# Kernel tuning notes

Measured on AMD Instinct MI355X. Metric: run time of the kernel, lower is better.

Reference implementation:

```python
import jax, jax.numpy as jnp
import numpy as np

N = 100_000   # nodes
E = 1_600_000 # edges (avg degree 16)
D0, D1, D2 = 128, 64, 64


def _linp(key, n_out, n_in):
    kw, kb = jax.random.split(key)
    s = 1.0 / np.sqrt(n_in)
    W = jax.random.uniform(kw, (n_out, n_in), jnp.float32, -s, s)
    b = jax.random.uniform(kb, (n_out,), jnp.float32, -s, s)
    return W, b


def setup_inputs() -> dict:
    key = jax.random.key(0)
    ks = jax.random.split(key, 9)
    h = jax.random.normal(ks[0], (N, D0), jnp.float32)
    # guarantee every row has at least one edge (avoids empty-row softmax / 0-std NaNs)
    rows = jnp.concatenate([jnp.arange(N, dtype=jnp.int32),
                            jax.random.randint(ks[1], (E - N,), 0, N, jnp.int32)])
    cols = jax.random.randint(ks[2], (E,), 0, N, jnp.int32)
    edge_index = jnp.stack([rows, cols])  # [2, E], row = softmax segment
    W11, b11 = _linp(ks[3], D1, D0)
    W12, b12 = _linp(ks[4], 1, D1)
    W13, b13 = _linp(ks[5], D1, D0)
    W21, b21 = _linp(ks[6], D2, D1)
    W22, b22 = _linp(ks[7], 1, D2)
    W23, b23 = _linp(ks[8], D2, D1)
    return dict(h=h, edge_index=edge_index,
                W11=W11, b11=b11, W12=W12, b12=b12, W13=W13, b13=b13,
                W21=W21, b21=b21, W22=W22, b22=b22, W23=W23, b23=b23)


def reference(h, edge_index, W11, b11, W12, b12, W13, b13,
              W21, b21, W22, b22, W23, b23):
    src, dst = edge_index[0], edge_index[1]

    def gat_layer(x, Wa, ba, We, be, Wv, bv):
        a = jnp.tanh(x @ Wa.T + ba)                       # [N, d] node scores (l11/l21)
        e = jnp.tanh((a[src] + a[dst]) @ We.T + be)[:, 0] # [E] per-edge logit (l12/l22)
        # per-row (segment) softmax over src = row index
        m = jax.ops.segment_max(e, src, num_segments=N)
        ex = jnp.exp(e - m[src])
        denom = jax.ops.segment_sum(ex, src, num_segments=N)
        att = ex / denom[src]                             # [E]
        v = jnp.tanh(x @ Wv.T + bv)                       # [N, d] values (l13/l23)
        out = jax.ops.segment_sum(att[:, None] * v[dst], src, num_segments=N)  # sparse mm
        return out / jnp.std(out, -1, keepdims=True, ddof=1)  # torch.std is unbiased

    h = gat_layer(h, W11, b11, W12, b12, W13, b13)
    h = gat_layer(h, W21, b21, W22, b22, W23, b23)
    return h
```

## Files before the change

kernel.cpp:

```cpp
#include <hip/hip_runtime.h>


#define WS_ALIGN 256
#define BIN_SHIFT 7
#define BIN_NODES 128
#define BIN_CAP 2560
#define MAX_BINS 1024
#define EPB 4096
#define AGGR_BLOCKS 2048

typedef __attribute__((ext_vector_type(8))) short short8;
typedef __attribute__((ext_vector_type(4))) float f32x4;

__device__ __forceinline__ float fast_tanh(float x) {
  x = fminf(15.f, fmaxf(-15.f, x));
  float e = __expf(2.f * x);
  return (e - 1.f) * __builtin_amdgcn_rcpf(e + 1.f);
}

__device__ __forceinline__ unsigned short f32_to_bf16_rne(float f) {
  unsigned u = __float_as_uint(f);
  unsigned r = u + 0x7fffu + ((u >> 16) & 1u);
  return (unsigned short)(r >> 16);
}

__device__ __forceinline__ void prepw_one(const float* __restrict__ Wa,
                                          const float* __restrict__ Wv,
                                          short* __restrict__ Wh, short* __restrict__ Wl,
                                          int K, int i) {
  int KBLK = K / 32;
  int j = i & 7;
  int c = (i >> 3) & 15;
  int q = (i >> 7) & 3;
  int r = i >> 9;
  int nt = r / KBLK, kb = r - nt * KBLK;
  int row = nt * 16 + c;
  int col = kb * 32 + q * 8 + j;
  float f = (row < 64) ? Wa[row * K + col] : Wv[(row - 64) * K + col];
  unsigned u = __float_as_uint(f);
  float hf = __uint_as_float(u & 0xffff0000u);
  Wh[i] = (short)(u >> 16);
  Wl[i] = (short)(__float_as_uint(f - hf) >> 16);
}

__global__ void k_setup(const float* __restrict__ W11, const float* __restrict__ W13,
                        short* __restrict__ Wh1, short* __restrict__ Wl1,
                        const float* __restrict__ W21, const float* __restrict__ W23,
                        short* __restrict__ Wh2, short* __restrict__ Wl2,
                        int* __restrict__ cursor, int nb) {
  int i = blockIdx.x * 256 + threadIdx.x;
  if (i < 16384) {
    prepw_one(W11, W13, Wh1, Wl1, 128, i);
  } else if (i < 16384 + 8192) {
    prepw_one(W21, W23, Wh2, Wl2, 64, i - 16384);
  } else {
    int b = i - 24576;
    if (b < nb) cursor[b] = b * BIN_CAP;
  }
}

__global__ __launch_bounds__(256) void k_bin(const int* __restrict__ src,
                                             const int* __restrict__ dst,
                                             int* __restrict__ cursor,
                                             int* __restrict__ binned, int E, int nb) {
  __shared__ int ssrc[EPB];
  __shared__ int sdst[EPB];
  __shared__ int hist[MAX_BINS];
  __shared__ int base[MAX_BINS];
  int t = threadIdx.x;
  for (int i = t; i < nb; i += 256) hist[i] = 0;
  __syncthreads();
  int e0 = blockIdx.x * EPB;
  for (int i = t; i < EPB; i += 256) {
    int e = e0 + i;
    int sv = -1, dv = 0;
    if (e < E) {
      sv = src[e];
      dv = dst[e];
      atomicAdd(&hist[sv >> BIN_SHIFT], 1);
    }
    ssrc[i] = sv;
    sdst[i] = dv;
  }
  __syncthreads();
  for (int b = t; b < nb; b += 256) {
    int c = hist[b];
    base[b] = c ? atomicAdd(&cursor[b], c) : 0;
    hist[b] = 0;
  }
  __syncthreads();
  for (int i = t; i < EPB; i += 256) {
    int sv = ssrc[i];
    if (sv >= 0) {
      int b = sv >> BIN_SHIFT;
      int r = atomicAdd(&hist[b], 1);
      int pos = base[b] + r;
      if (pos < (b + 1) * BIN_CAP)
        binned[pos] = (sdst[i] << BIN_SHIFT) | (sv & (BIN_NODES - 1));
    }
  }
}

__global__ __launch_bounds__(256) void k_sort_bin(int* __restrict__ binned,
                                                  const int* __restrict__ cursor,
                                                  int* __restrict__ rs,
                                                  int* __restrict__ re, int n) {
  __shared__ int ents[BIN_CAP];
  __shared__ int sorted[BIN_CAP];
  __shared__ int hist[BIN_NODES];
  __shared__ int scan[BIN_NODES];
  __shared__ int cur[BIN_NODES];
  int bin = blockIdx.x;
  int t = threadIdx.x;
  int nbase = bin << BIN_SHIFT;
  int cnt = cursor[bin] - bin * BIN_CAP;
  if (cnt > BIN_CAP) cnt = BIN_CAP;
  if (t < BIN_NODES) hist[t] = 0;
  __syncthreads();
  int* bp = binned + (size_t)bin * BIN_CAP;
  for (int i = t; i < cnt; i += 256) {
    int pk = bp[i];
    ents[i] = pk;
    atomicAdd(&hist[pk & (BIN_NODES - 1)], 1);
  }
  __syncthreads();
  if (t < BIN_NODES) scan[t] = hist[t];
  __syncthreads();
  for (int off = 1; off < BIN_NODES; off <<= 1) {
    int add = (t < BIN_NODES && t >= off) ? scan[t - off] : 0;
    __syncthreads();
    if (t < BIN_NODES) scan[t] += add;
    __syncthreads();
  }
  if (t < BIN_NODES) {
    int ex = scan[t] - hist[t];
    cur[t] = ex;
    int node = nbase + t;
    if (node < n) {
      rs[node] = bin * BIN_CAP + ex;
      re[node] = bin * BIN_CAP + ex + hist[t];
    }
  }
  __syncthreads();
  for (int i = t; i < cnt; i += 256) {
    int pk = ents[i];
    int pos = atomicAdd(&cur[pk & (BIN_NODES - 1)], 1);
    sorted[pos] = pk;
  }
  __syncthreads();
  for (int i = t; i < cnt; i += 256) {
    int pk = sorted[i];
    int node = pk & (BIN_NODES - 1);
    int hi = scan[node];
    int lo = hi - hist[node];
    int r = lo;
    for (int j = lo; j < hi; j++) {
      int pj = sorted[j];
      r += (pj < pk) || (pj == pk && j < i);
    }
    ents[r] = pk >> BIN_SHIFT;
  }
  __syncthreads();
  for (int i = t; i < cnt; i += 256) bp[i] = ents[i];
}

template <int K>
__global__ __launch_bounds__(256) void k_node(
    const float* __restrict__ x, const short* __restrict__ Wh,
    const short* __restrict__ Wl, const float* __restrict__ ba,
    const float* __restrict__ we, const float* __restrict__ bv,
    unsigned short* __restrict__ v_out, float* __restrict__ s_out, int n) {
  constexpr int KBLK = K / 32;
  constexpr int KP = K + 4;
  __shared__ float sx[64 * KP];
  int t = threadIdx.x;
  int l = t & 63;
  int w = t >> 6;
  int q = l >> 4, c = l & 15;
  int node0b = blockIdx.x * 64;

  {
    const float4* xg = (const float4*)(x + (size_t)node0b * K);
    constexpr int R4 = K / 4;
#pragma unroll
    for (int it = 0; it < 64 * R4 / 256; it++) {
      int i = it * 256 + t;
      int r = i / R4, k4 = i - r * R4;
      float4 val = (node0b + r < n) ? xg[i] : (float4){0.f, 0.f, 0.f, 0.f};
      *(float4*)&sx[r * KP + k4 * 4] = val;
    }
  }
  __syncthreads();

  int node0w = node0b + w * 16;
  if (node0w >= n) return;

  const short8* WhF = (const short8*)Wh;
  const short8* WlF = (const short8*)Wl;

  f32x4 acc[8];
#pragma unroll
  for (int i = 0; i < 8; i++) acc[i] = (f32x4){0.f, 0.f, 0.f, 0.f};

  const float* xl = sx + (w * 16 + c) * KP;

#pragma unroll 1
  for (int kb = 0; kb < KBLK; kb++) {
    float4 x0 = *(const float4*)&xl[kb * 32 + q * 8];
    float4 x1 = *(const float4*)&xl[kb * 32 + q * 8 + 4];
    float xv[8] = {x0.x, x0.y, x0.z, x0.w, x1.x, x1.y, x1.z, x1.w};
    short8 ah, al;
#pragma unroll
    for (int j = 0; j < 8; j++) {
      unsigned u = __float_as_uint(xv[j]);
      ah[j] = (short)(u >> 16);
      float hf = __uint_as_float(u & 0xffff0000u);
      al[j] = (short)(__float_as_uint(xv[j] - hf) >> 16);
    }
#pragma unroll
    for (int nt = 0; nt < 8; nt++) {
      short8 wh = WhF[(size_t)(nt * KBLK + kb) * 64 + l];
      short8 wl = WlF[(size_t)(nt * KBLK + kb) * 64 + l];
      acc[nt] = __builtin_amdgcn_mfma_f32_16x16x32_bf16(ah, wh, acc[nt], 0, 0, 0);
      acc[nt] = __builtin_amdgcn_mfma_f32_16x16x32_bf16(ah, wl, acc[nt], 0, 0, 0);
      acc[nt] = __builtin_amdgcn_mfma_f32_16x16x32_bf16(al, wh, acc[nt], 0, 0, 0);
    }
  }

  float p[4] = {0.f, 0.f, 0.f, 0.f};
#pragma unroll
  for (int nt = 0; nt < 4; nt++) {
    int o = nt * 16 + c;
    float bav = ba[o], wev = we[o];
#pragma unroll
    for (int r = 0; r < 4; r++) p[r] += fast_tanh(acc[nt][r] + bav) * wev;
  }
#pragma unroll
  for (int mm = 1; mm < 16; mm <<= 1) {
#pragma unroll
    for (int r = 0; r < 4; r++) p[r] += __shfl_xor(p[r], mm, 64);
  }
  if (c == 0) {
#pragma unroll
    for (int r = 0; r < 4; r++) {
      int node = node0w + q * 4 + r;
      if (node < n) s_out[node] = p[r];
    }
  }
#pragma unroll
  for (int nt = 4; nt < 8; nt++) {
    int o = (nt - 4) * 16 + c;
    float bvv = bv[o];
#pragma unroll
    for (int r = 0; r < 4; r++) {
      int node = node0w + q * 4 + r;
      if (node < n)
        v_out[(size_t)node * 64 + o] = f32_to_bf16_rne(fast_tanh(acc[nt][r] + bvv));
    }
  }
}

__global__ __launch_bounds__(256) void k_aggr(const int* __restrict__ rs,
                                              const int* __restrict__ re,
                                              const int* __restrict__ col,
                                              const float* __restrict__ s,
                                              const float* __restrict__ be_p,
                                              const unsigned short* __restrict__ v,
                                              float* __restrict__ out, int n) {
  int wid = (int)((blockIdx.x * 256 + threadIdx.x) >> 6);
  int nw = AGGR_BLOCKS * 4;
  int l = threadIdx.x & 63;
  int q = l >> 4;
  int g = l & 15;
  int qb = l & 48;
  float be = be_p[0];
  int ngroups = (n + 3) >> 2;

  for (int grp = wid; grp < ngroups; grp += nw) {
    int node = grp * 4 + q;
    bool vn = node < n;
    int e0 = vn ? rs[node] : 0;
    int e1 = vn ? re[node] : 0;
    float srow = vn ? s[node] : 0.f;
    float a0 = 0.f, a1 = 0.f, a2 = 0.f, a3 = 0.f;
    float dl = 0.f;

    for (int cb = 0;; cb += 16) {
      int rem = e1 - e0 - cb;
      if (__all(rem <= 0)) break;
      bool act = g < rem;
      int c = act ? col[e0 + cb + g] : 0;
      float w = act ? __expf(fast_tanh(srow + s[c] + be)) : 0.f;
      dl += w;
#pragma unroll
      for (int jj = 0; jj < 16; jj++) {
        int cj = __shfl(c, qb + jj, 64);
        float wj = __shfl(w, qb + jj, 64);
        uint2 pk = *(const uint2*)(v + ((size_t)cj << 6) + (g << 2));
        a0 = fmaf(wj, __uint_as_float(pk.x << 16), a0);
        a1 = fmaf(wj, __uint_as_float(pk.x & 0xffff0000u), a1);
        a2 = fmaf(wj, __uint_as_float(pk.y << 16), a2);
        a3 = fmaf(wj, __uint_as_float(pk.y & 0xffff0000u), a3);
      }
    }

#pragma unroll
    for (int mm = 1; mm < 16; mm <<= 1) dl += __shfl_xor(dl, mm, 64);
    float inv = __builtin_amdgcn_rcpf(dl);
    float o0 = a0 * inv, o1 = a1 * inv, o2 = a2 * inv, o3 = a3 * inv;
    float t0 = o0 + o1 + o2 + o3;
    float t1 = o0 * o0 + o1 * o1 + o2 * o2 + o3 * o3;
#pragma unroll
    for (int mm = 1; mm < 16; mm <<= 1) {
      t0 += __shfl_xor(t0, mm, 64);
      t1 += __shfl_xor(t1, mm, 64);
    }
    float var = (t1 - t0 * t0 * (1.0f / 64.f)) * (1.0f / 63.f);
    float isd = __builtin_amdgcn_rsqf(var);
    if (vn) {
      float4 r = {o0 * isd, o1 * isd, o2 * isd, o3 * isd};
      *(float4*)&out[(size_t)node * 64 + (g << 2)] = r;
    }
  }
}

extern "C" void kernel_launch(void* const* d_in, const int* in_sizes, int n_in,
                              void* d_out, int out_size, void* d_ws, size_t ws_size,
                              hipStream_t stream) {
  const float* h = (const float*)d_in[0];
  const int* ei = (const int*)d_in[1];
  const float* W11 = (const float*)d_in[2];
  const float* b11 = (const float*)d_in[3];
  const float* W12 = (const float*)d_in[4];
  const float* b12 = (const float*)d_in[5];
  const float* W13 = (const float*)d_in[6];
  const float* b13 = (const float*)d_in[7];
  const float* W21 = (const float*)d_in[8];
  const float* b21 = (const float*)d_in[9];
  const float* W22 = (const float*)d_in[10];
  const float* b22 = (const float*)d_in[11];
  const float* W23 = (const float*)d_in[12];
  const float* b23 = (const float*)d_in[13];

  const int N = in_sizes[0] / 128;
  const int E = in_sizes[1] / 2;
  const int* src = ei;
  const int* dst = ei + E;
  const int NB = (N + BIN_NODES - 1) >> BIN_SHIFT;

  char* p = (char*)d_ws;
  auto alloc = [&](size_t bytes) -> void* {
    void* r = (void*)p;
    p += (bytes + WS_ALIGN - 1) / WS_ALIGN * WS_ALIGN;
    return r;
  };
  int* cursor = (int*)alloc((size_t)NB * 4);
  int* binned = (int*)alloc((size_t)NB * BIN_CAP * 4);
  int* rsb = (int*)alloc((size_t)N * 4);
  int* reb = (int*)alloc((size_t)N * 4);
  float* sbuf = (float*)alloc((size_t)N * 4);
  unsigned short* vbuf = (unsigned short*)alloc((size_t)N * 64 * 2);
  float* out1 = (float*)alloc((size_t)N * 64 * 4);
  short* Wh1 = (short*)alloc(128 * 128 * 2);
  short* Wl1 = (short*)alloc(128 * 128 * 2);
  short* Wh2 = (short*)alloc(128 * 64 * 2);
  short* Wl2 = (short*)alloc(128 * 64 * 2);

  k_setup<<<(24576 + NB + 255) / 256, 256, 0, stream>>>(
      W11, W13, Wh1, Wl1, W21, W23, Wh2, Wl2, cursor, NB);

  k_bin<<<(E + EPB - 1) / EPB, 256, 0, stream>>>(src, dst, cursor, binned, E, NB);
  k_sort_bin<<<NB, 256, 0, stream>>>(binned, cursor, rsb, reb, N);

  k_node<128><<<(N + 63) / 64, 256, 0, stream>>>(h, Wh1, Wl1, b11, W12, b13, vbuf, sbuf, N);
  k_aggr<<<AGGR_BLOCKS, 256, 0, stream>>>(rsb, reb, binned, sbuf, b12, vbuf, out1, N);

  k_node<64><<<(N + 63) / 64, 256, 0, stream>>>(out1, Wh2, Wl2, b21, W22, b23, vbuf, sbuf, N);
  k_aggr<<<AGGR_BLOCKS, 256, 0, stream>>>(rsb, reb, binned, sbuf, b22, vbuf, (float*)d_out, N);
}
```

Baseline: 286.5 us.

## Restructure node GEMM with register-resident weights and prefetch next group in aggregation

The node kernel now splits fp32 inputs into bf16 hi/lo once while staging them to shared memory. Each wave keeps its slice of output-column weights in registers and loops over all 64 nodes, so weights are no longer reloaded from global memory per node tile. The score partials from two waves are combined through shared memory. The aggregation kernel software-pipelines the next group's row bounds, first column chunk and neighbor scores so their latency overlaps the current group's gather, at the cost of extra registers and a peeled first chunk.

```diff
diff --git a/kernel.cpp b/kernel.cpp
--- a/kernel.cpp
+++ b/kernel.cpp
@@ -10,6 +10,7 @@
 #define AGGR_BLOCKS 2048
 
 typedef __attribute__((ext_vector_type(8))) short short8;
+typedef __attribute__((ext_vector_type(4))) short short4_t;
 typedef __attribute__((ext_vector_type(4))) float f32x4;
 
 __device__ __forceinline__ float fast_tanh(float x) {
@@ -171,8 +172,10 @@
     const float* __restrict__ we, const float* __restrict__ bv,
     unsigned short* __restrict__ v_out, float* __restrict__ s_out, int n) {
   constexpr int KBLK = K / 32;
-  constexpr int KP = K + 4;
-  __shared__ float sx[64 * KP];
+  constexpr int RS = K + 8;
+  __shared__ short sah[64 * RS];
+  __shared__ short sal[64 * RS];
+  __shared__ float sP[2][64];
   int t = threadIdx.x;
   int l = t & 63;
   int w = t >> 6;
@@ -187,76 +190,90 @@
       int i = it * 256 + t;
       int r = i / R4, k4 = i - r * R4;
       float4 val = (node0b + r < n) ? xg[i] : (float4){0.f, 0.f, 0.f, 0.f};
-      *(float4*)&sx[r * KP + k4 * 4] = val;
-    }
-  }
-  __syncthreads();
-
-  int node0w = node0b + w * 16;
-  if (node0w >= n) return;
+      float xv[4] = {val.x, val.y, val.z, val.w};
+      short4_t hi, lo;
+#pragma unroll
+      for (int j = 0; j < 4; j++) {
+        unsigned u = __float_as_uint(xv[j]);
+        hi[j] = (short)(u >> 16);
+        float hf = __uint_as_float(u & 0xffff0000u);
+        lo[j] = (short)(__float_as_uint(xv[j] - hf) >> 16);
+      }
+      *(short4_t*)&sah[r * RS + k4 * 4] = hi;
+      *(short4_t*)&sal[r * RS + k4 * 4] = lo;
+    }
+  }
 
   const short8* WhF = (const short8*)Wh;
   const short8* WlF = (const short8*)Wl;
-
-  f32x4 acc[8];
-#pragma unroll
-  for (int i = 0; i < 8; i++) acc[i] = (f32x4){0.f, 0.f, 0.f, 0.f};
-
-  const float* xl = sx + (w * 16 + c) * KP;
-
-#pragma unroll 1
-  for (int kb = 0; kb < KBLK; kb++) {
-    float4 x0 = *(const float4*)&xl[kb * 32 + q * 8];
-    float4 x1 = *(const float4*)&xl[kb * 32 + q * 8 + 4];
-    float xv[8] = {x0.x, x0.y, x0.z, x0.w, x1.x, x1.y, x1.z, x1.w};
-    short8 ah, al;
-#pragma unroll
-    for (int j = 0; j < 8; j++) {
-      unsigned u = __float_as_uint(xv[j]);
-      ah[j] = (short)(u >> 16);
-      float hf = __uint_as_float(u & 0xffff0000u);
-      al[j] = (short)(__float_as_uint(xv[j] - hf) >> 16);
-    }
-#pragma unroll
-    for (int nt = 0; nt < 8; nt++) {
-      short8 wh = WhF[(size_t)(nt * KBLK + kb) * 64 + l];
-      short8 wl = WlF[(size_t)(nt * KBLK + kb) * 64 + l];
-      acc[nt] = __builtin_amdgcn_mfma_f32_16x16x32_bf16(ah, wh, acc[nt], 0, 0, 0);
-      acc[nt] = __builtin_amdgcn_mfma_f32_16x16x32_bf16(ah, wl, acc[nt], 0, 0, 0);
-      acc[nt] = __builtin_amdgcn_mfma_f32_16x16x32_bf16(al, wh, acc[nt], 0, 0, 0);
-    }
-  }
-
-  float p[4] = {0.f, 0.f, 0.f, 0.f};
-#pragma unroll
-  for (int nt = 0; nt < 4; nt++) {
-    int o = nt * 16 + c;
-    float bav = ba[o], wev = we[o];
-#pragma unroll
-    for (int r = 0; r < 4; r++) p[r] += fast_tanh(acc[nt][r] + bav) * wev;
-  }
-#pragma unroll
-  for (int mm = 1; mm < 16; mm <<= 1) {
-#pragma unroll
-    for (int r = 0; r < 4; r++) p[r] += __shfl_xor(p[r], mm, 64);
-  }
-  if (c == 0) {
-#pragma unroll
-    for (int r = 0; r < 4; r++) {
-      int node = node0w + q * 4 + r;
-      if (node < n) s_out[node] = p[r];
-    }
-  }
-#pragma unroll
-  for (int nt = 4; nt < 8; nt++) {
-    int o = (nt - 4) * 16 + c;
-    float bvv = bv[o];
-#pragma unroll
-    for (int r = 0; r < 4; r++) {
-      int node = node0w + q * 4 + r;
-      if (node < n)
-        v_out[(size_t)node * 64 + o] = f32_to_bf16_rne(fast_tanh(acc[nt][r] + bvv));
-    }
+  short8 wfh[2][KBLK], wfl[2][KBLK];
+#pragma unroll
+  for (int mt = 0; mt < 2; mt++)
+#pragma unroll
+    for (int kb = 0; kb < KBLK; kb++) {
+      size_t f = (size_t)((2 * w + mt) * KBLK + kb) * 64 + l;
+      wfh[mt][kb] = WhF[f];
+      wfl[mt][kb] = WlF[f];
+    }
+  __syncthreads();
+
+  f32x4 acc[4][2];
+#pragma unroll
+  for (int ns = 0; ns < 4; ns++)
+#pragma unroll
+    for (int mt = 0; mt < 2; mt++) acc[ns][mt] = (f32x4){0.f, 0.f, 0.f, 0.f};
+
+#pragma unroll
+  for (int ns = 0; ns < 4; ns++) {
+#pragma unroll
+    for (int kb = 0; kb < KBLK; kb++) {
+      int off = (ns * 16 + c) * RS + kb * 32 + q * 8;
+      short8 ah = *(const short8*)&sah[off];
+      short8 al = *(const short8*)&sal[off];
+#pragma unroll
+      for (int mt = 0; mt < 2; mt++) {
+        acc[ns][mt] = __builtin_amdgcn_mfma_f32_16x16x32_bf16(ah, wfh[mt][kb], acc[ns][mt], 0, 0, 0);
+        acc[ns][mt] = __builtin_amdgcn_mfma_f32_16x16x32_bf16(ah, wfl[mt][kb], acc[ns][mt], 0, 0, 0);
+        acc[ns][mt] = __builtin_amdgcn_mfma_f32_16x16x32_bf16(al, wfh[mt][kb], acc[ns][mt], 0, 0, 0);
+      }
+    }
+  }
+
+  if (w < 2) {
+    float bav0 = ba[w * 32 + c], wev0 = we[w * 32 + c];
+    float bav1 = ba[w * 32 + 16 + c], wev1 = we[w * 32 + 16 + c];
+#pragma unroll
+    for (int ns = 0; ns < 4; ns++) {
+#pragma unroll
+      for (int r = 0; r < 4; r++) {
+        float pv = fast_tanh(acc[ns][0][r] + bav0) * wev0 +
+                   fast_tanh(acc[ns][1][r] + bav1) * wev1;
+#pragma unroll
+        for (int mm = 1; mm < 16; mm <<= 1) pv += __shfl_xor(pv, mm, 64);
+        if (c == 0) sP[w][ns * 16 + q * 4 + r] = pv;
+      }
+    }
+  } else {
+    int wv = w - 2;
+    float bvv0 = bv[wv * 32 + c], bvv1 = bv[wv * 32 + 16 + c];
+#pragma unroll
+    for (int ns = 0; ns < 4; ns++) {
+#pragma unroll
+      for (int r = 0; r < 4; r++) {
+        int node = node0b + ns * 16 + q * 4 + r;
+        if (node < n) {
+          v_out[(size_t)node * 64 + wv * 32 + c] =
+              f32_to_bf16_rne(fast_tanh(acc[ns][0][r] + bvv0));
+          v_out[(size_t)node * 64 + wv * 32 + 16 + c] =
+              f32_to_bf16_rne(fast_tanh(acc[ns][1][r] + bvv1));
+        }
+      }
+    }
+  }
+  __syncthreads();
+  if (t < 64) {
+    int node = node0b + t;
+    if (node < n) s_out[node] = sP[0][t] + sP[1][t];
   }
 }
 
@@ -275,20 +292,59 @@
   int qb = l & 48;
   float be = be_p[0];
   int ngroups = (n + 3) >> 2;
+  if (wid >= ngroups) return;
+
+  int pnode = wid * 4 + q;
+  bool pvn = pnode < n;
+  int pe0 = pvn ? rs[pnode] : 0;
+  int pe1 = pvn ? re[pnode] : 0;
+  float psrow = pvn ? s[pnode] : 0.f;
+  int pc;
+  float psc;
+  {
+    int prem = pe1 - pe0;
+    pc = (g < prem) ? col[pe0 + g] : 0;
+    psc = (g < prem) ? s[pc] : 0.f;
+  }
 
   for (int grp = wid; grp < ngroups; grp += nw) {
-    int node = grp * 4 + q;
-    bool vn = node < n;
-    int e0 = vn ? rs[node] : 0;
-    int e1 = vn ? re[node] : 0;
-    float srow = vn ? s[node] : 0.f;
+    int e0 = pe0, e1 = pe1;
+    float srow = psrow;
+    int c0 = pc;
+    float sc0 = psc;
+    int nxt = grp + nw;
+    if (nxt < ngroups) {
+      int nn = nxt * 4 + q;
+      bool nv = nn < n;
+      pe0 = nv ? rs[nn] : 0;
+      pe1 = nv ? re[nn] : 0;
+      psrow = nv ? s[nn] : 0.f;
+    }
+    int m = e1 - e0;
     float a0 = 0.f, a1 = 0.f, a2 = 0.f, a3 = 0.f;
     float dl = 0.f;
 
-    for (int cb = 0;; cb += 16) {
-      int rem = e1 - e0 - cb;
-      if (__all(rem <= 0)) break;
-      bool act = g < rem;
+    {
+      float w = (g < m) ? __expf(fast_tanh(srow + sc0 + be)) : 0.f;
+      dl += w;
+#pragma unroll
+      for (int jj = 0; jj < 16; jj++) {
+        int cj = __shfl(c0, qb + jj, 64);
+        float wj = __shfl(w, qb + jj, 64);
+        uint2 pk = *(const uint2*)(v + ((size_t)cj << 6) + (g << 2));
+        a0 = fmaf(wj, __uint_as_float(pk.x << 16), a0);
+        a1 = fmaf(wj, __uint_as_float(pk.x & 0xffff0000u), a1);
+        a2 = fmaf(wj, __uint_as_float(pk.y << 16), a2);
+        a3 = fmaf(wj, __uint_as_float(pk.y & 0xffff0000u), a3);
+      }
+    }
+    if (nxt < ngroups) {
+      int nrem = pe1 - pe0;
+      pc = (g < nrem) ? col[pe0 + g] : 0;
+      psc = (g < nrem) ? s[pc] : 0.f;
+    }
+    for (int cb = 16; !__all(m - cb <= 0); cb += 16) {
+      bool act = (cb + g) < m;
       int c = act ? col[e0 + cb + g] : 0;
       float w = act ? __expf(fast_tanh(srow + s[c] + be)) : 0.f;
       dl += w;
@@ -317,9 +373,10 @@
     }
     float var = (t1 - t0 * t0 * (1.0f / 64.f)) * (1.0f / 63.f);
     float isd = __builtin_amdgcn_rsqf(var);
-    if (vn) {
+    int cnode = grp * 4 + q;
+    if (cnode < n) {
       float4 r = {o0 * isd, o1 * isd, o2 * isd, o3 * isd};
-      *(float4*)&out[(size_t)node * 64 + (g << 2)] = r;
+      *(float4*)&out[(size_t)cnode * 64 + (g << 2)] = r;
     }
   }
 }
```

New measurement: 280.4 us. 2.1% less time.
